# Kernel tuning notes

Hardware: AMD Instinct MI355X
Metric: run time of the kernel (lower is better)

## Reference

```python
import jax, jax.numpy as jnp
import numpy as np

N, E, F = 50000, 800000, 64


def _lin_init(key, fan_in, fan_out):
    k1, k2 = jax.random.split(key)
    bound = 1.0 / np.sqrt(fan_in)
    W = jax.random.uniform(k1, (fan_in, fan_out), minval=-bound, maxval=bound, dtype=jnp.float32)
    b = jax.random.uniform(k2, (fan_out,), minval=-bound, maxval=bound, dtype=jnp.float32)
    return W, b


def setup_inputs() -> dict:
    key = jax.random.key(0)
    ks = jax.random.split(key, 16)
    inp = {
        'node_attr': jax.random.normal(ks[0], (N, 3), dtype=jnp.float32),
        'edge_attr': jax.random.normal(ks[1], (E, 3), dtype=jnp.float32),
        'edge_index': jax.random.randint(ks[2], (2, E), 0, N, dtype=jnp.int32),
    }
    # conv1: in = 2*3 + 3 = 9
    inp['c1_W1'], inp['c1_b1'] = _lin_init(ks[3], 9, F)
    inp['c1_W2'], inp['c1_b2'] = _lin_init(ks[4], F, F)
    # conv2: in = 2*F + (F + 3)
    inp['c2_W1'], inp['c2_b1'] = _lin_init(ks[5], 2 * F + F + 3, F)
    inp['c2_W2'], inp['c2_b2'] = _lin_init(ks[6], F, F)
    # conv3/conv4: in = 2*(2F) + 2F = 6F
    inp['c3_W1'], inp['c3_b1'] = _lin_init(ks[7], 6 * F, F)
    inp['c3_W2'], inp['c3_b2'] = _lin_init(ks[8], F, F)
    inp['c4_W1'], inp['c4_b1'] = _lin_init(ks[9], 6 * F, F)
    inp['c4_W2'], inp['c4_b2'] = _lin_init(ks[10], F, F)
    # head mlp: F -> 64 -> 3
    inp['m_W1'], inp['m_b1'] = _lin_init(ks[11], F, 64)
    inp['m_W2'], inp['m_b2'] = _lin_init(ks[12], 64, 3)
    return inp


def _edge_conv(x, row, col, e_attr, W1, b1, W2, b2):
    # gather -> concat -> 2-layer MLP on edges
    h = jnp.concatenate([x[row], x[col], e_attr], axis=1)  # [E, 2*Dn + De]
    edge_out = jax.nn.relu(h @ W1 + b1) @ W2 + b2          # [E, F]
    # scatter-mean back to source nodes
    s = jax.ops.segment_sum(edge_out, row, num_segments=x.shape[0])
    cnt = jax.ops.segment_sum(jnp.ones((row.shape[0],), edge_out.dtype), row, num_segments=x.shape[0])
    node_out = s / jnp.maximum(cnt, 1.0)[:, None]
    return node_out, edge_out


def reference(node_attr, edge_attr, edge_index,
              c1_W1, c1_b1, c1_W2, c1_b2,
              c2_W1, c2_b1, c2_W2, c2_b2,
              c3_W1, c3_b1, c3_W2, c3_b2,
              c4_W1, c4_b1, c4_W2, c4_b2,
              m_W1, m_b1, m_W2, m_b2):
    row, col = edge_index[0], edge_index[1]
    relu = jax.nn.relu

    x1, e1 = _edge_conv(node_attr, row, col, edge_attr, c1_W1, c1_b1, c1_W2, c1_b2)
    x1, e1 = relu(x1), relu(e1)

    x2, e2 = _edge_conv(x1, row, col, jnp.concatenate([e1, edge_attr], axis=1),
                        c2_W1, c2_b1, c2_W2, c2_b2)
    x2, e2 = relu(x2), relu(e2)

    x_ll, x_l = x1, x2
    e_ll, e_l = e1, e2
    for (W1, b1, W2, b2) in ((c3_W1, c3_b1, c3_W2, c3_b2), (c4_W1, c4_b1, c4_W2, c4_b2)):
        x_cur, e_cur = _edge_conv(jnp.concatenate([x_l, x_ll], axis=1), row, col,
                                  jnp.concatenate([e_l, e_ll], axis=1), W1, b1, W2, b2)
        x_cur, e_cur = relu(x_cur), relu(e_cur)
        x_ll, x_l = x_l, x_cur
        e_ll, e_l = e_l, e_cur

    x = relu(x_l @ m_W1 + m_b1) @ m_W2 + m_b2  # [N, 3]
    return (x, e_l)
```

## Files before the change

kernel.cpp:

```cpp
#include <hip/hip_runtime.h>
#include <cstdint>
#include <cstddef>


#define NN 50000
#define NE 800000

typedef _Float16 f16;
typedef _Float16 f16x8 __attribute__((ext_vector_type(8)));
typedef _Float16 f16x4 __attribute__((ext_vector_type(4)));
typedef float    f32x4 __attribute__((ext_vector_type(4)));

__global__ void count_kernel(const int* __restrict__ eidx, int* __restrict__ cnt) {
  int i = blockIdx.x * 256 + threadIdx.x;
  if (i < NE) atomicAdd(&cnt[eidx[i]], 1);
}

__global__ void scan_a(const int* __restrict__ cnt, int* __restrict__ bsum) {
  __shared__ int sh[256];
  int i = blockIdx.x * 256 + threadIdx.x;
  sh[threadIdx.x] = (i < NN) ? cnt[i] : 0;
  __syncthreads();
  for (int off = 128; off > 0; off >>= 1) {
    if (threadIdx.x < off) sh[threadIdx.x] += sh[threadIdx.x + off];
    __syncthreads();
  }
  if (threadIdx.x == 0) bsum[blockIdx.x] = sh[0];
}

__global__ void scan_b(const int* __restrict__ bsum, int* __restrict__ boff, int nb) {
  __shared__ int sh[256];
  int t = threadIdx.x;
  int v = (t < nb) ? bsum[t] : 0;
  sh[t] = v; __syncthreads();
  for (int off = 1; off < 256; off <<= 1) {
    int x = (t >= off) ? sh[t - off] : 0;
    __syncthreads();
    sh[t] += x;
    __syncthreads();
  }
  if (t < nb) boff[t] = sh[t] - v;
}

__global__ void scan_c(const int* __restrict__ cnt, const int* __restrict__ boff,
                       int* __restrict__ start, int* __restrict__ cursor) {
  __shared__ int sh[256];
  int t = threadIdx.x;
  int i = blockIdx.x * 256 + t;
  int v = (i < NN) ? cnt[i] : 0;
  sh[t] = v; __syncthreads();
  for (int off = 1; off < 256; off <<= 1) {
    int x = (t >= off) ? sh[t - off] : 0;
    __syncthreads();
    sh[t] += x;
    __syncthreads();
  }
  if (i < NN) {
    int ex = boff[blockIdx.x] + sh[t] - v;
    start[i] = ex; cursor[i] = ex;
  }
  if (i == 0) start[NN] = NE;
}

__global__ void scatter_kernel(const int* __restrict__ eidx, const float* __restrict__ ea,
                               int* __restrict__ cursor,
                               int* __restrict__ srow, int* __restrict__ scol,
                               int* __restrict__ perm, f16* __restrict__ ea4) {
  int e = blockIdx.x * 256 + threadIdx.x;
  if (e >= NE) return;
  int r = eidx[e];
  int j = atomicAdd(&cursor[r], 1);
  srow[j] = r;
  scol[j] = eidx[NE + e];
  perm[j] = e;
  f16x4 v;
  v[0] = (f16)ea[3 * (size_t)e];
  v[1] = (f16)ea[3 * (size_t)e + 1];
  v[2] = (f16)ea[3 * (size_t)e + 2];
  v[3] = (f16)0.0f;
  *(f16x4*)&ea4[4 * (size_t)j] = v;
}

__global__ void prep_kernel(const float* __restrict__ W1, int kreal1, int ksteps1,
                            int ident_ks, int koff,
                            const float* __restrict__ W2,
                            f16* __restrict__ w1f, f16* __restrict__ w2f) {
  int u = blockIdx.x * 256 + threadIdx.x;
  int total1 = ksteps1 * 256;
  if (u < total1) {
    int slot = u;
    int l = slot & 63, t = (slot >> 6) & 3, ks = slot >> 8;
    int n = t * 16 + (l & 15);
    f16x8 v;
    if (ks < ident_ks) {
#pragma unroll
      for (int j = 0; j < 8; ++j) {
        int lk = (ks & 1) * 32 + ((l >> 4) * 8) + j;
        v[j] = (lk == n) ? (f16)1.0f : (f16)0.0f;
      }
    } else {
      int kb = koff + (ks - ident_ks) * 32 + ((l >> 4) * 8);
#pragma unroll
      for (int j = 0; j < 8; ++j) {
        int k = kb + j;
        v[j] = (f16)((k < kreal1) ? W1[k * 64 + n] : 0.0f);
      }
    }
    *(f16x8*)&w1f[slot * 8] = v;
  } else if (u < total1 + 512) {
    int slot = u - total1;
    int l = slot & 63, t = (slot >> 6) & 3, ks = slot >> 8;
    int n = t * 16 + (l & 15);
    int kb = ks * 32 + ((l >> 4) * 8);
    f16x8 v;
#pragma unroll
    for (int j = 0; j < 8; ++j)
      v[j] = (f16)W2[(kb + j) * 64 + n];
    *(f16x8*)&w2f[slot * 8] = v;
  }
}

__global__ __launch_bounds__(256, 2) void node_proj_kernel(
    const f16* __restrict__ xA, const f16* __restrict__ xB,
    const f16* __restrict__ w1p,
    f16* __restrict__ fN, f16* __restrict__ gN)
{
  __shared__ f16 wps[8 * 2048];
  __shared__ __align__(16) f16 hbuf[4][16][40];
  const int tid  = threadIdx.x;
  const int lane = tid & 63;
  const int wv   = tid >> 6;
  const int quad = lane >> 4;
  const int l15  = lane & 15;

  for (int u = tid; u < 8 * 256; u += 256)
    *(f16x8*)&wps[u * 8] = *(const f16x8*)&w1p[u * 8];
  __syncthreads();

  constexpr int NT = (NN + 31) / 32;
  const int stride = gridDim.x * 4;
  for (int tI = blockIdx.x * 4 + wv; tI < NT; tI += stride) {
    const int nb = tI * 32;
    const int m0 = nb + l15, m1 = nb + 16 + l15;
    const size_t n0 = (size_t)(m0 < NN ? m0 : NN - 1);
    const size_t n1 = (size_t)(m1 < NN ? m1 : NN - 1);
    f16x8 a0[4], a1[4];
#pragma unroll
    for (int ks = 0; ks < 4; ++ks) {
      const f16* src = (ks < 2) ? xA : xB;
      const int kk = ks & 1;
      a0[ks] = *(const f16x8*)(src + n0 * 64 + kk * 32 + quad * 8);
      a1[ks] = *(const f16x8*)(src + n1 * 64 + kk * 32 + quad * 8);
    }
    f32x4 af[2][4], ag[2][4];
#pragma unroll
    for (int s = 0; s < 2; ++s)
#pragma unroll
      for (int t = 0; t < 4; ++t) {
        af[s][t] = (f32x4){0.f, 0.f, 0.f, 0.f};
        ag[s][t] = (f32x4){0.f, 0.f, 0.f, 0.f};
      }
#pragma unroll
    for (int ks = 0; ks < 4; ++ks) {
#pragma unroll
      for (int t = 0; t < 4; ++t) {
        f16x8 bf = *(const f16x8*)&wps[((ks * 4 + t) * 64 + lane) * 8];
        f16x8 bg = *(const f16x8*)&wps[(((4 + ks) * 4 + t) * 64 + lane) * 8];
        af[0][t] = __builtin_amdgcn_mfma_f32_16x16x32_f16(a0[ks], bf, af[0][t], 0, 0, 0);
        af[1][t] = __builtin_amdgcn_mfma_f32_16x16x32_f16(a1[ks], bf, af[1][t], 0, 0, 0);
        ag[0][t] = __builtin_amdgcn_mfma_f32_16x16x32_f16(a0[ks], bg, ag[0][t], 0, 0, 0);
        ag[1][t] = __builtin_amdgcn_mfma_f32_16x16x32_f16(a1[ks], bg, ag[1][t], 0, 0, 0);
      }
    }
#pragma unroll
    for (int s = 0; s < 2; ++s) {
      const int row = nb + s * 16 + l15;
      f16x8 oh[2];
#pragma unroll
      for (int h = 0; h < 2; ++h) {
#pragma unroll
        for (int th = 0; th < 2; ++th) {
          const int t = h * 2 + th;
#pragma unroll
          for (int r = 0; r < 4; ++r)
            hbuf[wv][quad * 4 + r][th * 16 + l15] = (f16)af[s][t][r];
        }
        oh[h] = *(const f16x8*)&hbuf[wv][l15][quad * 8];
      }
      if (row < NN) {
        *(f16x8*)&fN[(size_t)row * 64 + quad * 8] = oh[0];
        *(f16x8*)&fN[(size_t)row * 64 + 32 + quad * 8] = oh[1];
      }
#pragma unroll
      for (int h = 0; h < 2; ++h) {
#pragma unroll
        for (int th = 0; th < 2; ++th) {
          const int t = h * 2 + th;
#pragma unroll
          for (int r = 0; r < 4; ++r)
            hbuf[wv][quad * 4 + r][th * 16 + l15] = (f16)ag[s][t][r];
        }
        oh[h] = *(const f16x8*)&hbuf[wv][l15][quad * 8];
      }
      if (row < NN) {
        *(f16x8*)&gN[(size_t)row * 64 + quad * 8] = oh[0];
        *(f16x8*)&gN[(size_t)row * 64 + 32 + quad * 8] = oh[1];
      }
    }
  }
}

template<int F32OUT>
__global__ void node_sum_kernel(const f16* __restrict__ eout, const int* __restrict__ start,
                                void* __restrict__ xout) {
  int v = blockIdx.x * 4 + (threadIdx.x >> 6);
  int lane = threadIdx.x & 63;
  int g = lane >> 4, c4 = (lane & 15) * 4;
  int s0 = start[v], s1 = start[v + 1];
  f32x4 acc = (f32x4){0.f, 0.f, 0.f, 0.f};
  for (int i = s0 + g; i < s1; i += 4) {
    f16x4 h = *(const f16x4*)&eout[(size_t)i * 64 + c4];
#pragma unroll
    for (int q = 0; q < 4; ++q) acc[q] += (float)h[q];
  }
#pragma unroll
  for (int q = 0; q < 4; ++q) {
    acc[q] += __shfl_xor(acc[q], 16, 64);
    acc[q] += __shfl_xor(acc[q], 32, 64);
  }
  int cv = s1 - s0;
  float inv = 1.0f / (float)(cv > 0 ? cv : 1);
  if (g == 0) {
    if (F32OUT) {
      f32x4 o;
#pragma unroll
      for (int q = 0; q < 4; ++q) o[q] = fmaxf(acc[q] * inv, 0.0f);
      *(f32x4*)&((float*)xout)[(size_t)v * 64 + c4] = o;
    } else {
      f16x4 o;
#pragma unroll
      for (int q = 0; q < 4; ++q) o[q] = (f16)fmaxf(acc[q] * inv, 0.0f);
      *(f16x4*)&((f16*)xout)[(size_t)v * 64 + c4] = o;
    }
  }
}

template<int CONV>
__global__ __launch_bounds__(256, 2) void edge_conv_kernel(
    const int* __restrict__ srow, const int* __restrict__ scol,
    const int* __restrict__ perm,
    const float* __restrict__ na,
    const f16* __restrict__ xA, const f16* __restrict__ xB,
    const f16* __restrict__ eA, const f16* __restrict__ eB,
    const f16* __restrict__ ea4,
    const f16* __restrict__ w1f, const f16* __restrict__ w2f,
    const float* __restrict__ b1, const float* __restrict__ b2,
    f16* __restrict__ eout, float* __restrict__ out_e)
{
  constexpr int KSTEPS = (CONV == 1) ? 1 : (CONV == 2 ? 7 : 8);

  __shared__ f16 w1s[KSTEPS * 2048];
  __shared__ __align__(16) f16 hbuf[4][16][40];

  const int tid  = threadIdx.x;
  const int lane = tid & 63;
  const int wv   = tid >> 6;
  const int quad = lane >> 4;
  const int l15  = lane & 15;

  for (int u = tid; u < KSTEPS * 256; u += 256)
    *(f16x8*)&w1s[u * 8] = *(const f16x8*)&w1f[u * 8];

  float bb1[4], bb2[4];
#pragma unroll
  for (int t = 0; t < 4; ++t) { bb1[t] = b1[t * 16 + l15]; bb2[t] = b2[t * 16 + l15]; }

  f16x8 w2r[2][4];
#pragma unroll
  for (int kk = 0; kk < 2; ++kk)
#pragma unroll
    for (int t = 0; t < 4; ++t)
      w2r[kk][t] = *(const f16x8*)&w2f[((kk * 4 + t) * 64 + lane) * 8];

  __syncthreads();

  constexpr int NTILE = NE / 32;
  const int gw = blockIdx.x * 4 + wv;
  const int stride = gridDim.x * 4;

  auto epilogue = [&](f32x4 (&acc)[2][4], int jb) {
#pragma unroll
    for (int s = 0; s < 2; ++s) {
      f32x4 a2[4];
#pragma unroll
      for (int t = 0; t < 4; ++t) a2[t] = (f32x4){0.f, 0.f, 0.f, 0.f};
#pragma unroll
      for (int kk = 0; kk < 2; ++kk) {
#pragma unroll
        for (int th = 0; th < 2; ++th) {
          const int t = kk * 2 + th;
#pragma unroll
          for (int r = 0; r < 4; ++r)
            hbuf[wv][quad * 4 + r][th * 16 + l15] = (f16)fmaxf(acc[s][t][r] + bb1[t], 0.0f);
        }
        f16x8 ah = *(const f16x8*)&hbuf[wv][l15][quad * 8];
#pragma unroll
        for (int t = 0; t < 4; ++t)
          a2[t] = __builtin_amdgcn_mfma_f32_16x16x32_f16(ah, w2r[kk][t], a2[t], 0, 0, 0);
      }

      const int j = jb + s * 16 + l15;
      f16x8 oh[2];
#pragma unroll
      for (int h = 0; h < 2; ++h) {
#pragma unroll
        for (int th = 0; th < 2; ++th) {
          const int t = h * 2 + th;
#pragma unroll
          for (int r = 0; r < 4; ++r)
            hbuf[wv][quad * 4 + r][th * 16 + l15] = (f16)(a2[t][r] + bb2[t]);
        }
        oh[h] = *(const f16x8*)&hbuf[wv][l15][quad * 8];
      }
      *(f16x8*)&eout[(size_t)j * 64 + quad * 8] = oh[0];
      *(f16x8*)&eout[(size_t)j * 64 + 32 + quad * 8] = oh[1];

      if constexpr (CONV == 4) {
#pragma unroll
        for (int r = 0; r < 4; ++r) {
          const int p = perm[jb + s * 16 + quad * 4 + r];
#pragma unroll
          for (int t = 0; t < 4; ++t)
            out_e[(size_t)p * 64 + t * 16 + l15] = fmaxf(a2[t][r] + bb2[t], 0.0f);
        }
      }
    }
  };

  if constexpr (CONV == 1) {
    for (int jt = gw; jt < NTILE; jt += stride) {
      const int jb = jt * 32;
      const int j0 = jb + l15, j1 = j0 + 16;
      const int r0 = srow[j0], r1 = srow[j1];
      const int c0 = scol[j0], c1 = scol[j1];
      f16x8 a0, a1;
#pragma unroll
      for (int j = 0; j < 8; ++j) { a0[j] = (f16)0.0f; a1[j] = (f16)0.0f; }
      f16x4 q0 = *(const f16x4*)&ea4[4 * (size_t)j0];
      f16x4 q1 = *(const f16x4*)&ea4[4 * (size_t)j1];
      if (quad == 0) {
        a0[0] = (f16)na[r0*3];  a0[1] = (f16)na[r0*3+1];  a0[2] = (f16)na[r0*3+2];
        a0[3] = (f16)na[c0*3];  a0[4] = (f16)na[c0*3+1];  a0[5] = (f16)na[c0*3+2];
        a0[6] = q0[0];          a0[7] = q0[1];
        a1[0] = (f16)na[r1*3];  a1[1] = (f16)na[r1*3+1];  a1[2] = (f16)na[r1*3+2];
        a1[3] = (f16)na[c1*3];  a1[4] = (f16)na[c1*3+1];  a1[5] = (f16)na[c1*3+2];
        a1[6] = q1[0];          a1[7] = q1[1];
      } else if (quad == 1) {
        a0[0] = q0[2];
        a1[0] = q1[2];
      }
      f32x4 acc[2][4];
#pragma unroll
      for (int s = 0; s < 2; ++s)
#pragma unroll
        for (int t = 0; t < 4; ++t) acc[s][t] = (f32x4){0.f, 0.f, 0.f, 0.f};
#pragma unroll
      for (int t = 0; t < 4; ++t) {
        f16x8 b = *(const f16x8*)&w1s[(t * 64 + lane) * 8];
        acc[0][t] = __builtin_amdgcn_mfma_f32_16x16x32_f16(a0, b, acc[0][t], 0, 0, 0);
        acc[1][t] = __builtin_amdgcn_mfma_f32_16x16x32_f16(a1, b, acc[1][t], 0, 0, 0);
      }
      epilogue(acc, jb);
    }
  } else {
    constexpr int NREG = (CONV == 2) ? 3 : 4;
    constexpr int ERCH = 2;

    int jt = gw;
    int pr0 = 0, pr1 = 0, pc0 = 0, pc1 = 0;
    if (jt < NTILE) {
      const int jb = jt * 32;
      pr0 = srow[jb + l15];  pr1 = srow[jb + 16 + l15];
      pc0 = scol[jb + l15];  pc1 = scol[jb + 16 + l15];
    }

    for (; jt < NTILE; jt += stride) {
      const int jb = jt * 32;
      const int j0 = jb + l15, j1 = j0 + 16;

      const int jn = jt + stride;
      int nr0 = 0, nr1 = 0, nc0 = 0, nc1 = 0;
      if (jn < NTILE) {
        const int njb = jn * 32;
        nr0 = srow[njb + l15];  nr1 = srow[njb + 16 + l15];
        nc0 = scol[njb + l15];  nc1 = scol[njb + 16 + l15];
      }

      const int r0 = pr0, r1 = pr1, c0 = pc0, c1 = pc1;
      const f16* p0[NREG]; const f16* p1[NREG];
      if constexpr (CONV == 2) {
        p0[0] = xA + (size_t)r0 * 64;  p1[0] = xA + (size_t)r1 * 64;
        p0[1] = xA + (size_t)c0 * 64;  p1[1] = xA + (size_t)c1 * 64;
        p0[2] = eA + (size_t)j0 * 64;  p1[2] = eA + (size_t)j1 * 64;
      } else {
        p0[0] = xA + (size_t)r0 * 64;  p1[0] = xA + (size_t)r1 * 64;
        p0[1] = xB + (size_t)c0 * 64;  p1[1] = xB + (size_t)c1 * 64;
        p0[2] = eA + (size_t)j0 * 64;  p1[2] = eA + (size_t)j1 * 64;
        p0[3] = eB + (size_t)j0 * 64;  p1[3] = eB + (size_t)j1 * 64;
      }

      f32x4 acc[2][4];
#pragma unroll
      for (int s = 0; s < 2; ++s)
#pragma unroll
        for (int t = 0; t < 4; ++t) acc[s][t] = (f32x4){0.f, 0.f, 0.f, 0.f};

#pragma unroll
      for (int ks = 0; ks < NREG * 2; ++ks) {
        const int c = ks >> 1, kk = ks & 1;
        f16x8 a0 = *(const f16x8*)(p0[c] + kk * 32 + quad * 8);
        f16x8 a1 = *(const f16x8*)(p1[c] + kk * 32 + quad * 8);
        if (c >= ERCH) {
#pragma unroll
          for (int j = 0; j < 8; ++j) {
            a0[j] = (a0[j] > (f16)0.0f) ? a0[j] : (f16)0.0f;
            a1[j] = (a1[j] > (f16)0.0f) ? a1[j] : (f16)0.0f;
          }
        }
#pragma unroll
        for (int t = 0; t < 4; ++t) {
          if constexpr (CONV >= 3) {
            if (ks < 4 && ((ks & 1) ? (t < 2) : (t >= 2))) continue;
          }
          f16x8 b = *(const f16x8*)&w1s[((ks * 4 + t) * 64 + lane) * 8];
          acc[0][t] = __builtin_amdgcn_mfma_f32_16x16x32_f16(a0, b, acc[0][t], 0, 0, 0);
          acc[1][t] = __builtin_amdgcn_mfma_f32_16x16x32_f16(a1, b, acc[1][t], 0, 0, 0);
        }
      }
      if constexpr (CONV == 2) {
        f16x8 a0, a1;
#pragma unroll
        for (int j = 0; j < 8; ++j) { a0[j] = (f16)0.0f; a1[j] = (f16)0.0f; }
        f16x4 q0 = *(const f16x4*)&ea4[4 * (size_t)j0];
        f16x4 q1 = *(const f16x4*)&ea4[4 * (size_t)j1];
        if (quad == 0) {
          a0[0] = q0[0]; a0[1] = q0[1]; a0[2] = q0[2];
          a1[0] = q1[0]; a1[1] = q1[1]; a1[2] = q1[2];
        }
#pragma unroll
        for (int t = 0; t < 4; ++t) {
          f16x8 b = *(const f16x8*)&w1s[((6 * 4 + t) * 64 + lane) * 8];
          acc[0][t] = __builtin_amdgcn_mfma_f32_16x16x32_f16(a0, b, acc[0][t], 0, 0, 0);
          acc[1][t] = __builtin_amdgcn_mfma_f32_16x16x32_f16(a1, b, acc[1][t], 0, 0, 0);
        }
      }

      epilogue(acc, jb);

      pr0 = nr0; pr1 = nr1; pc0 = nc0; pc1 = nc1;
    }
  }
}

__global__ void head_kernel(const float* __restrict__ x4,
                            const float* __restrict__ W1, const float* __restrict__ b1,
                            const float* __restrict__ W2, const float* __restrict__ b2,
                            float* __restrict__ out) {
  __shared__ float xs[4][64];
  __shared__ float hs[4][64];
  int tid = threadIdx.x;
  int i = tid >> 6, f = tid & 63;
  int nb = blockIdx.x * 4;
  xs[i][f] = x4[(size_t)(nb + i) * 64 + f];
  __syncthreads();
  float h = b1[f];
#pragma unroll
  for (int k = 0; k < 64; ++k) h += xs[i][k] * W1[k * 64 + f];
  hs[i][f] = fmaxf(h, 0.0f);
  __syncthreads();
  if (tid < 12) {
    int ii = tid / 3, j = tid % 3;
    float o = b2[j];
#pragma unroll
    for (int k = 0; k < 64; ++k) o += hs[ii][k] * W2[k * 3 + j];
    out[(size_t)(nb + ii) * 3 + j] = o;
  }
}

extern "C" void kernel_launch(void* const* d_in, const int* in_sizes, int n_in,
                              void* d_out, int out_size, void* d_ws, size_t ws_size,
                              hipStream_t stream) {
  const float* na   = (const float*)d_in[0];
  const float* ea   = (const float*)d_in[1];
  const int*   eidx = (const int*)d_in[2];
  const float* c1W1 = (const float*)d_in[3];
  const float* c1b1 = (const float*)d_in[4];
  const float* c1W2 = (const float*)d_in[5];
  const float* c1b2 = (const float*)d_in[6];
  const float* c2W1 = (const float*)d_in[7];
  const float* c2b1 = (const float*)d_in[8];
  const float* c2W2 = (const float*)d_in[9];
  const float* c2b2 = (const float*)d_in[10];
  const float* c3W1 = (const float*)d_in[11];
  const float* c3b1 = (const float*)d_in[12];
  const float* c3W2 = (const float*)d_in[13];
  const float* c3b2 = (const float*)d_in[14];
  const float* c4W1 = (const float*)d_in[15];
  const float* c4b1 = (const float*)d_in[16];
  const float* c4W2 = (const float*)d_in[17];
  const float* c4b2 = (const float*)d_in[18];
  const float* mW1  = (const float*)d_in[19];
  const float* mb1  = (const float*)d_in[20];
  const float* mW2  = (const float*)d_in[21];
  const float* mb2  = (const float*)d_in[22];

  char* ws = (char*)d_ws;
  size_t off = 0;
  auto alloc = [&](size_t b) -> void* {
    void* p = ws + off;
    off += (b + 255) & ~(size_t)255;
    return p;
  };
  int*   cnt    = (int*)alloc((size_t)NN * 4);
  int*   bsum   = (int*)alloc(256 * 4);
  int*   boff   = (int*)alloc(256 * 4);
  int*   start  = (int*)alloc((size_t)(NN + 1) * 4);
  int*   cursor = (int*)alloc((size_t)NN * 4);
  int*   srow   = (int*)alloc((size_t)NE * 4);
  int*   scol   = (int*)alloc((size_t)NE * 4);
  int*   perm   = (int*)alloc((size_t)NE * 4);
  f16*   ea4    = (f16*)alloc((size_t)NE * 4 * 2);
  f16*   x1     = (f16*)alloc((size_t)NN * 64 * 2);
  f16*   x2     = (f16*)alloc((size_t)NN * 64 * 2);
  f16*   x3     = (f16*)alloc((size_t)NN * 64 * 2);
  float* x4     = (float*)alloc((size_t)NN * 64 * 4);
  f16*   fN3    = (f16*)alloc((size_t)NN * 64 * 2);
  f16*   gN3    = (f16*)alloc((size_t)NN * 64 * 2);
  f16*   fN4    = (f16*)alloc((size_t)NN * 64 * 2);
  f16*   gN4    = (f16*)alloc((size_t)NN * 64 * 2);
  f16*   se1    = (f16*)alloc((size_t)NE * 64 * 2);
  f16*   se2    = (f16*)alloc((size_t)NE * 64 * 2);
  f16*   se3    = (f16*)alloc((size_t)NE * 64 * 2);
  f16*   w1f1 = (f16*)alloc((size_t) 1 * 2048 * 2);
  f16*   w1f2 = (f16*)alloc((size_t) 7 * 2048 * 2);
  f16*   w1f3 = (f16*)alloc((size_t) 8 * 2048 * 2);
  f16*   w1f4 = (f16*)alloc((size_t) 8 * 2048 * 2);
  f16*   w1p3 = (f16*)alloc((size_t) 8 * 2048 * 2);
  f16*   w1p4 = (f16*)alloc((size_t) 8 * 2048 * 2);
  f16*   w2f1 = (f16*)alloc((size_t)4096 * 2);
  f16*   w2f2 = (f16*)alloc((size_t)4096 * 2);
  f16*   w2f3 = (f16*)alloc((size_t)4096 * 2);
  f16*   w2f4 = (f16*)alloc((size_t)4096 * 2);

  float* out_x = (float*)d_out;
  float* out_e = out_x + (size_t)NN * 3;

  constexpr int NBS = (NN + 255) / 256;
  constexpr int GRID_EC = 1024;
  constexpr int GRID_NP = 391;

  hipMemsetAsync(cnt, 0, (size_t)NN * 4, stream);
  count_kernel<<<NE / 256, 256, 0, stream>>>(eidx, cnt);
  scan_a<<<NBS, 256, 0, stream>>>(cnt, bsum);
  scan_b<<<1, 256, 0, stream>>>(bsum, boff, NBS);
  scan_c<<<NBS, 256, 0, stream>>>(cnt, boff, start, cursor);
  scatter_kernel<<<NE / 256, 256, 0, stream>>>(eidx, ea, cursor, srow, scol, perm, ea4);

  prep_kernel<<< 3, 256, 0, stream>>>(c1W1,   9, 1, 0,   0, c1W2, w1f1, w2f1);
  prep_kernel<<< 9, 256, 0, stream>>>(c2W1, 195, 7, 0,   0, c2W2, w1f2, w2f2);
  prep_kernel<<<10, 256, 0, stream>>>(c3W1, 384, 8, 4, 256, c3W2, w1f3, w2f3);
  prep_kernel<<<10, 256, 0, stream>>>(c4W1, 384, 8, 4, 256, c4W2, w1f4, w2f4);
  prep_kernel<<<10, 256, 0, stream>>>(c3W1, 384, 8, 0,   0, c3W2, w1p3, w2f3);
  prep_kernel<<<10, 256, 0, stream>>>(c4W1, 384, 8, 0,   0, c4W2, w1p4, w2f4);

  edge_conv_kernel<1><<<GRID_EC, 256, 0, stream>>>(srow, scol, nullptr, na,
      nullptr, nullptr, nullptr, nullptr, ea4, w1f1, w2f1, c1b1, c1b2, se1, nullptr);
  node_sum_kernel<0><<<NN / 4, 256, 0, stream>>>(se1, start, x1);

  edge_conv_kernel<2><<<GRID_EC, 256, 0, stream>>>(srow, scol, nullptr, nullptr,
      x1, nullptr, se1, nullptr, ea4, w1f2, w2f2, c2b1, c2b2, se2, nullptr);
  node_sum_kernel<0><<<NN / 4, 256, 0, stream>>>(se2, start, x2);

  node_proj_kernel<<<GRID_NP, 256, 0, stream>>>(x2, x1, w1p3, fN3, gN3);
  edge_conv_kernel<3><<<GRID_EC, 256, 0, stream>>>(srow, scol, nullptr, nullptr,
      fN3, gN3, se2, se1, nullptr, w1f3, w2f3, c3b1, c3b2, se3, nullptr);
  node_sum_kernel<0><<<NN / 4, 256, 0, stream>>>(se3, start, x3);

  node_proj_kernel<<<GRID_NP, 256, 0, stream>>>(x3, x2, w1p4, fN4, gN4);
  edge_conv_kernel<4><<<GRID_EC, 256, 0, stream>>>(srow, scol, perm, nullptr,
      fN4, gN4, se3, se2, nullptr, w1f4, w2f4, c4b1, c4b2, se1, out_e);
  node_sum_kernel<1><<<NN / 4, 256, 0, stream>>>(se1, start, x4);

  head_kernel<<<NN / 4, 256, 0, stream>>>(x4, mW1, mb1, mW2, mb2, out_x);
}
```

Measured before the change: 864.7 us.

## Fuse final-layer scatter-sum into edge conv via segmented atomics

In the last edge convolution the kernel no longer writes the f16 edge output buffer. It reduces consecutive same-source edges within each 16-edge group using ballot and shuffles, then atomically adds the partial sums into a zeroed f32 node accumulator. A small finalize kernel then divides by the degree and applies ReLU. This removes the edge output write and the node_sum pass that re-reads it, at the cost of a memset, float atomics and extra shuffle work in the epilogue.

```diff
diff --git a/kernel.cpp b/kernel.cpp
--- a/kernel.cpp
+++ b/kernel.cpp
@@ -245,6 +245,16 @@
   }
 }
 
+__global__ void finalize_x_kernel(float* __restrict__ x4, const int* __restrict__ start) {
+  int tid = threadIdx.x;
+  int v = blockIdx.x * 4 + (tid >> 6);
+  int c = tid & 63;
+  int cv = start[v + 1] - start[v];
+  float inv = 1.0f / (float)(cv > 0 ? cv : 1);
+  float val = x4[(size_t)v * 64 + c];
+  x4[(size_t)v * 64 + c] = fmaxf(val * inv, 0.0f);
+}
+
 template<int CONV>
 __global__ __launch_bounds__(256, 2) void edge_conv_kernel(
     const int* __restrict__ srow, const int* __restrict__ scol,
@@ -255,7 +265,8 @@
     const f16* __restrict__ ea4,
     const f16* __restrict__ w1f, const f16* __restrict__ w2f,
     const float* __restrict__ b1, const float* __restrict__ b2,
-    f16* __restrict__ eout, float* __restrict__ out_e)
+    f16* __restrict__ eout, float* __restrict__ out_e,
+    float* __restrict__ xacc)
 {
   constexpr int KSTEPS = (CONV == 1) ? 1 : (CONV == 2 ? 7 : 8);
 
@@ -288,7 +299,7 @@
   const int gw = blockIdx.x * 4 + wv;
   const int stride = gridDim.x * 4;
 
-  auto epilogue = [&](f32x4 (&acc)[2][4], int jb) {
+  auto epilogue = [&](f32x4 (&acc)[2][4], int jb, int rs0, int rs1) {
 #pragma unroll
     for (int s = 0; s < 2; ++s) {
       f32x4 a2[4];
@@ -309,29 +320,59 @@
           a2[t] = __builtin_amdgcn_mfma_f32_16x16x32_f16(ah, w2r[kk][t], a2[t], 0, 0, 0);
       }
 
-      const int j = jb + s * 16 + l15;
-      f16x8 oh[2];
-#pragma unroll
-      for (int h = 0; h < 2; ++h) {
-#pragma unroll
-        for (int th = 0; th < 2; ++th) {
-          const int t = h * 2 + th;
-#pragma unroll
-          for (int r = 0; r < 4; ++r)
-            hbuf[wv][quad * 4 + r][th * 16 + l15] = (f16)(a2[t][r] + bb2[t]);
-        }
-        oh[h] = *(const f16x8*)&hbuf[wv][l15][quad * 8];
-      }
-      *(f16x8*)&eout[(size_t)j * 64 + quad * 8] = oh[0];
-      *(f16x8*)&eout[(size_t)j * 64 + 32 + quad * 8] = oh[1];
-
-      if constexpr (CONV == 4) {
+      if constexpr (CONV != 4) {
+        const int j = jb + s * 16 + l15;
+        f16x8 oh[2];
+#pragma unroll
+        for (int h = 0; h < 2; ++h) {
+#pragma unroll
+          for (int th = 0; th < 2; ++th) {
+            const int t = h * 2 + th;
+#pragma unroll
+            for (int r = 0; r < 4; ++r)
+              hbuf[wv][quad * 4 + r][th * 16 + l15] = (f16)(a2[t][r] + bb2[t]);
+          }
+          oh[h] = *(const f16x8*)&hbuf[wv][l15][quad * 8];
+        }
+        *(f16x8*)&eout[(size_t)j * 64 + quad * 8] = oh[0];
+        *(f16x8*)&eout[(size_t)j * 64 + 32 + quad * 8] = oh[1];
+      } else {
 #pragma unroll
         for (int r = 0; r < 4; ++r) {
           const int p = perm[jb + s * 16 + quad * 4 + r];
 #pragma unroll
           for (int t = 0; t < 4; ++t)
             out_e[(size_t)p * 64 + t * 16 + l15] = fmaxf(a2[t][r] + bb2[t], 0.0f);
+        }
+        const int myv = (s == 0) ? rs0 : rs1;
+        const int pv  = __shfl(myv, (l15 > 0) ? (l15 - 1) : 0, 64);
+        const bool sf = (l15 == 0) || (myv != pv);
+        unsigned long long starts = __ballot(sf) & 0xFFFFull;
+        while (starts) {
+          const int a = __builtin_ctzll(starts);
+          starts &= starts - 1;
+          const int b = starts ? __builtin_ctzll(starts) : 16;
+          const int va = __shfl(myv, a, 64);
+          float sm[4];
+#pragma unroll
+          for (int t = 0; t < 4; ++t) {
+            sm[t] = 0.f;
+#pragma unroll
+            for (int r = 0; r < 4; ++r) {
+              const int w = quad * 4 + r;
+              sm[t] += (w >= a && w < b) ? (a2[t][r] + bb2[t]) : 0.0f;
+            }
+          }
+#pragma unroll
+          for (int t = 0; t < 4; ++t) {
+            sm[t] += __shfl_xor(sm[t], 16, 64);
+            sm[t] += __shfl_xor(sm[t], 32, 64);
+          }
+          if (quad == 0) {
+#pragma unroll
+            for (int t = 0; t < 4; ++t)
+              atomicAdd(&xacc[(size_t)va * 64 + t * 16 + l15], sm[t]);
+          }
         }
       }
     }
@@ -370,7 +411,7 @@
         acc[0][t] = __builtin_amdgcn_mfma_f32_16x16x32_f16(a0, b, acc[0][t], 0, 0, 0);
         acc[1][t] = __builtin_amdgcn_mfma_f32_16x16x32_f16(a1, b, acc[1][t], 0, 0, 0);
       }
-      epilogue(acc, jb);
+      epilogue(acc, jb, r0, r1);
     }
   } else {
     constexpr int NREG = (CONV == 2) ? 3 : 4;
@@ -455,7 +496,7 @@
         }
       }
 
-      epilogue(acc, jb);
+      epilogue(acc, jb, r0, r1);
 
       pr0 = nr0; pr1 = nr1; pc0 = nc0; pc1 = nc1;
     }
@@ -560,6 +601,7 @@
   constexpr int GRID_NP = 391;
 
   hipMemsetAsync(cnt, 0, (size_t)NN * 4, stream);
+  hipMemsetAsync(x4, 0, (size_t)NN * 64 * 4, stream);
   count_kernel<<<NE / 256, 256, 0, stream>>>(eidx, cnt);
   scan_a<<<NBS, 256, 0, stream>>>(cnt, bsum);
   scan_b<<<1, 256, 0, stream>>>(bsum, boff, NBS);
@@ -574,22 +616,26 @@
   prep_kernel<<<10, 256, 0, stream>>>(c4W1, 384, 8, 0,   0, c4W2, w1p4, w2f4);
 
   edge_conv_kernel<1><<<GRID_EC, 256, 0, stream>>>(srow, scol, nullptr, na,
-      nullptr, nullptr, nullptr, nullptr, ea4, w1f1, w2f1, c1b1, c1b2, se1, nullptr);
+      nullptr, nullptr, nullptr, nullptr, ea4, w1f1, w2f1, c1b1, c1b2, se1, nullptr,
+      nullptr);
   node_sum_kernel<0><<<NN / 4, 256, 0, stream>>>(se1, start, x1);
 
   edge_conv_kernel<2><<<GRID_EC, 256, 0, stream>>>(srow, scol, nullptr, nullptr,
-      x1, nullptr, se1, nullptr, ea4, w1f2, w2f2, c2b1, c2b2, se2, nullptr);
+      x1, nullptr, se1, nullptr, ea4, w1f2, w2f2, c2b1, c2b2, se2, nullptr,
+      nullptr);
   node_sum_kernel<0><<<NN / 4, 256, 0, stream>>>(se2, start, x2);
 
   node_proj_kernel<<<GRID_NP, 256, 0, stream>>>(x2, x1, w1p3, fN3, gN3);
   edge_conv_kernel<3><<<GRID_EC, 256, 0, stream>>>(srow, scol, nullptr, nullptr,
-      fN3, gN3, se2, se1, nullptr, w1f3, w2f3, c3b1, c3b2, se3, nullptr);
+      fN3, gN3, se2, se1, nullptr, w1f3, w2f3, c3b1, c3b2, se3, nullptr,
+      nullptr);
   node_sum_kernel<0><<<NN / 4, 256, 0, stream>>>(se3, start, x3);
 
   node_proj_kernel<<<GRID_NP, 256, 0, stream>>>(x3, x2, w1p4, fN4, gN4);
   edge_conv_kernel<4><<<GRID_EC, 256, 0, stream>>>(srow, scol, perm, nullptr,
-      fN4, gN4, se3, se2, nullptr, w1f4, w2f4, c4b1, c4b2, se1, out_e);
-  node_sum_kernel<1><<<NN / 4, 256, 0, stream>>>(se1, start, x4);
+      fN4, gN4, se3, se2, nullptr, w1f4, w2f4, c4b1, c4b2, nullptr, out_e,
+      x4);
+  finalize_x_kernel<<<NN / 4, 256, 0, stream>>>(x4, start);
 
   head_kernel<<<NN / 4, 256, 0, stream>>>(x4, mW1, mb1, mW2, mb2, out_x);
 }
```

Result: faster. 830.6 us (-3.9%).
